# Performance work log

Hardware: AMD Instinct MI355X
Metric: run time of the kernel (lower is better)

Reference implementation:

```python
import jax, jax.numpy as jnp
import numpy as np

B, LQ, LF, NW, NFR, E, D, V = 4, 128, 64, 2, 8, 128, 128, 64


def _project(x, W, b):
    # torch Emb_Projection('linear'): Linear then zero-row mask
    y = x @ W + b
    m = 1.0 - jnp.all(y == 0, axis=-1, keepdims=True).astype(y.dtype)
    return y * m


def setup_inputs() -> dict:
    key = jax.random.key(0)
    ks = jax.random.split(key, 12)
    s = lambda k, shape, fan: jax.random.normal(k, shape, jnp.float32) / np.sqrt(fan)
    return {
        "query": jax.random.normal(ks[0], (B, LQ, E), jnp.float32),
        "fragment": jax.random.normal(ks[1], (B, NW, NFR, LF, E), jnp.float32),
        "query_mask": jnp.ones((B, LQ), jnp.float32),
        "fragment_mask": jnp.ones((B, NW, NFR, LF), jnp.float32),
        # learned params (stored [in, out]; torch Linear is x @ W.T with W [out,in])
        "proj_W": s(ks[2], (E, D), E),
        "proj_b": jnp.zeros((D,), jnp.float32),
        "self_att_W": s(ks[3], (NW, D), D),   # n_way Linear(D,1,bias=False)
        "q_att_W": s(ks[4], (D, V), D),
        "f_att_W": s(ks[5], (D, V), D),
        "qf_att_W": s(ks[6], (D, V), D),
        "gate_w": s(ks[7], (V,), V),          # value_gate: Linear(V,1,bias=False)
        "val_w": s(ks[8], (V,), V),           # value_att:  Linear(V,1,bias=False)
    }


def reference(query, fragment, query_mask, fragment_mask, proj_W, proj_b,
              self_att_W, q_att_W, f_att_W, qf_att_W, gate_w, val_w):
    query = _project(query, proj_W, proj_b)          # [B,Lq,D]
    fragment = _project(fragment, proj_W, proj_b)    # [B,NW,NFR,Lf,D]

    # (1) fragment self-attention -> frag_code
    logits = jnp.einsum('bwfld,wd->bwfl', fragment, self_att_W)   # per-way Linear(D,1)
    e = jnp.exp(logits) * fragment_mask
    frag_self_att = e / (e.sum(-1, keepdims=True) + 1e-7)          # [B,NW,NFR,Lf]
    frag_code = (fragment * frag_self_att[..., None]).sum(-2)     # [B,NW,NFR,D]

    # (2) query-to-fragment attention
    frag_r = fragment.reshape(fragment.shape[0], -1, fragment.shape[-2], fragment.shape[-1])  # [B,NF,Lf,D]
    qr = query[:, None]                                            # [B,1,Lq,D]
    q_att = qr @ q_att_W                                           # [B,1,Lq,V]
    f_att = frag_r @ f_att_W                                       # [B,NF,Lf,V]
    # large broadcast product [B,NF,Lf,Lq,D] then project to V
    qf = (qr[:, :, None, :, :] * frag_r[:, :, :, None, :]) @ qf_att_W  # [B,NF,Lf,Lq,V]
    qf = q_att[:, :, None] + f_att[:, :, :, None] + qf
    qf = qf.max(axis=-3)                                           # max over Lf -> [B,NF,Lq,V]

    qf_gate = jax.nn.sigmoid(qf @ gate_w) * query_mask[:, None]    # [B,NF,Lq]
    e2 = jnp.exp(qf @ val_w) * query_mask[:, None]
    qf_norm = e2 / (e2.sum(-1, keepdims=True) + 1e-7)              # [B,NF,Lq]

    query_code = (qr * qf_norm[..., None]).sum(axis=2)             # [B,NF,D]
    query_code = query_code.reshape(frag_code.shape)               # [B,NW,NFR,D]
    return frag_code, query_code, frag_self_att, qf_gate, query
```

## Files before the change

### kernel.cpp

```cpp
#include <hip/hip_runtime.h>
#include <hip/hip_bf16.h>

#define B_   4
#define LQ_  128
#define LF_  64
#define NW_  2
#define NFR_ 8
#define E_   128
#define D_   128
#define V_   64
#define NWF_ (NW_*NFR_)

using bf16 = __hip_bfloat16;
typedef unsigned short u16;
typedef unsigned int   u32;
typedef __attribute__((ext_vector_type(8))) short  bf16x8;
typedef __attribute__((ext_vector_type(4))) float  f32x4;
typedef __attribute__((ext_vector_type(4))) u32    u32x4;

#define OUT_FRAGCODE  0
#define OUT_QUERYCODE 8192
#define OUT_SELFATT   16384
#define OUT_QFGATE    20480
#define OUT_QUERY     28672

#define L_FP   0
#define L_QP   16384
#define L_FA   49152
#define L_E2   58368
#define L_N    58880
#define L_SAW  59392
#define L_ATT  59904
#define L_RED  60160
#define L_PART 62208
#define L_TOT  62240

__device__ __forceinline__ float us2f(u16 v) { return __uint_as_float((u32)v << 16); }
__device__ __forceinline__ float lo2f(u32 v) { return __uint_as_float(v << 16); }
__device__ __forceinline__ float hi2f(u32 v) { return __uint_as_float(v & 0xffff0000u); }
__device__ __forceinline__ u16 f2b_raw(float f) {
    u32 u = __float_as_uint(f);
    return (u16)((u + 0x7fffu + ((u >> 16) & 1u)) >> 16);
}
__device__ __forceinline__ u32 pk2(float hi, float lo) {
    return __builtin_amdgcn_perm(__float_as_uint(hi), __float_as_uint(lo), 0x07060302u);
}
template<bool BF> __device__ __forceinline__ float LD(const void* p, int i) {
    return BF ? us2f(((const u16*)p)[i]) : ((const float*)p)[i];
}
template<bool BF> __device__ __forceinline__ void ST(void* p, int i, float v) {
    if (BF) ((u16*)p)[i] = f2b_raw(v); else ((float*)p)[i] = v;
}
template<bool BF> __device__ __forceinline__ u16 LDB(const void* p, int i) {
    return BF ? ((const u16*)p)[i] : f2b_raw(((const float*)p)[i]);
}
__device__ __forceinline__ bool is_bf(const void* qmask) {
    return ((const u16*)qmask)[0] == 0x3F80u;
}
template<bool BF>
__device__ __forceinline__ bf16x8 loadA(const void* x, int row, int kt, int quad) {
    int off = row * 128 + kt * 32 + quad * 8;
    if (BF) return *(const bf16x8*)((const u16*)x + off);
    f32x4 a = *(const f32x4*)((const float*)x + off);
    f32x4 c = *(const f32x4*)((const float*)x + off + 4);
    u32x4 av;
    av.x = pk2(a.y, a.x); av.y = pk2(a.w, a.z);
    av.z = pk2(c.y, c.x); av.w = pk2(c.w, c.z);
    return __builtin_bit_cast(bf16x8, av);
}
template<bool BF>
__device__ __forceinline__ bf16x8 ldBf(const void* W, int N, int n, int k0) {
    short tmp[8];
    #pragma unroll
    for (int j = 0; j < 8; ++j) tmp[j] = (short)LDB<BF>(W, (k0 + j) * N + n);
    bf16x8 f;
    #pragma unroll
    for (int j = 0; j < 8; ++j) f[j] = tmp[j];
    return f;
}

template<bool BF>
__device__ __forceinline__ void main_body(
    const void* query, const void* fragment, const void* qmask, const void* fmask,
    const void* projW, const void* projB, const void* saW, const void* qattW,
    const void* fattW, const void* qfW, const void* gatew, const void* valw,
    void* out, char* smem)
{
    u16*   s_fp   = (u16*)(smem + L_FP);
    u16*   s_qp   = (u16*)(smem + L_QP);
    u16*   s_fa   = (u16*)(smem + L_FA);
    float* s_e2   = (float*)(smem + L_E2);
    float* s_n    = (float*)(smem + L_N);
    float* s_saw  = (float*)(smem + L_SAW);
    float* s_att  = (float*)(smem + L_ATT);
    float* s_red  = (float*)(smem + L_RED);
    float* s_part = (float*)(smem + L_PART);

    int bwf = blockIdx.x, b = bwf >> 4;
    int t = threadIdx.x, lane = t & 63, w = t >> 6;
    int m = lane & 15, quad = lane >> 4;
    int sk = (m & 7) << 3;

    {
        bool dofp = (w < 4);
        bf16x8 af_q[4], af_f[4];
        #pragma unroll
        for (int kt = 0; kt < 4; ++kt)
            af_q[kt] = loadA<BF>(query, b * 128 + w * 16 + m, kt, quad);
        if (dofp)
            #pragma unroll
            for (int kt = 0; kt < 4; ++kt)
                af_f[kt] = loadA<BF>(fragment, bwf * 64 + w * 16 + m, kt, quad);
        #pragma unroll
        for (int nt = 0; nt < 8; ++nt) {
            int n = nt * 16 + m;
            bf16x8 bw[4];
            #pragma unroll
            for (int kt = 0; kt < 4; ++kt) bw[kt] = ldBf<BF>(projW, 128, n, kt * 32 + quad * 8);
            float bv = LD<BF>(projB, n);
            f32x4 aq = (f32x4){bv, bv, bv, bv};
            #pragma unroll
            for (int kt = 0; kt < 4; ++kt)
                aq = __builtin_amdgcn_mfma_f32_16x16x32_bf16(af_q[kt], bw[kt], aq, 0, 0, 0);
            #pragma unroll
            for (int rr = 0; rr < 4; ++rr) {
                int row = w * 16 + quad * 4 + rr;
                s_qp[row * 128 + (n ^ ((row & 7) << 3))] = f2b_raw(aq[rr]);
            }
            if (dofp) {
                f32x4 afc = (f32x4){bv, bv, bv, bv};
                #pragma unroll
                for (int kt = 0; kt < 4; ++kt)
                    afc = __builtin_amdgcn_mfma_f32_16x16x32_bf16(af_f[kt], bw[kt], afc, 0, 0, 0);
                #pragma unroll
                for (int rr = 0; rr < 4; ++rr) {
                    int row = w * 16 + quad * 4 + rr;
                    s_fp[row * 128 + (n ^ ((row & 7) << 3))] = f2b_raw(afc[rr]);
                }
            }
        }
    }
    __syncthreads();

    bf16x8 aq2[4];
    #pragma unroll
    for (int kt = 0; kt < 4; ++kt)
        aq2[kt] = *(const bf16x8*)&s_qp[(w * 16 + m) * 128 + ((kt * 32 + quad * 8) ^ sk)];
    f32x4 qat[4];
    #pragma unroll
    for (int vt = 0; vt < 4; ++vt) {
        qat[vt] = (f32x4){0.f, 0.f, 0.f, 0.f};
        #pragma unroll
        for (int kt = 0; kt < 4; ++kt) {
            bf16x8 bb = ldBf<BF>(qattW, 64, vt * 16 + m, kt * 32 + quad * 8);
            qat[vt] = __builtin_amdgcn_mfma_f32_16x16x32_bf16(aq2[kt], bb, qat[vt], 0, 0, 0);
        }
    }
    float qpreg[4][8];
    #pragma unroll
    for (int kt = 0; kt < 4; ++kt) {
        u32x4 uv = __builtin_bit_cast(u32x4, aq2[kt]);
        qpreg[kt][0] = lo2f(uv.x); qpreg[kt][1] = hi2f(uv.x);
        qpreg[kt][2] = lo2f(uv.y); qpreg[kt][3] = hi2f(uv.y);
        qpreg[kt][4] = lo2f(uv.z); qpreg[kt][5] = hi2f(uv.z);
        qpreg[kt][6] = lo2f(uv.w); qpreg[kt][7] = hi2f(uv.w);
    }
    if (w < 4) {
        bf16x8 afa[4];
        #pragma unroll
        for (int kt = 0; kt < 4; ++kt)
            afa[kt] = *(const bf16x8*)&s_fp[(w * 16 + m) * 128 + ((kt * 32 + quad * 8) ^ sk)];
        #pragma unroll
        for (int vt = 0; vt < 4; ++vt) {
            f32x4 a0 = (f32x4){0.f, 0.f, 0.f, 0.f};
            #pragma unroll
            for (int kt = 0; kt < 4; ++kt) {
                bf16x8 wk = ldBf<BF>(fattW, 64, vt * 16 + m, kt * 32 + quad * 8);
                a0 = __builtin_amdgcn_mfma_f32_16x16x32_bf16(afa[kt], wk, a0, 0, 0, 0);
            }
            #pragma unroll
            for (int r = 0; r < 4; ++r)
                s_fa[(w * 16 + quad * 4 + r) * 72 + vt * 16 + m] = f2b_raw(a0[r]);
        }
    }
    bf16x8 w3f[4][4];
    #pragma unroll
    for (int vt = 0; vt < 4; ++vt)
        #pragma unroll
        for (int kt = 0; kt < 4; ++kt)
            w3f[vt][kt] = ldBf<BF>(qfW, 64, vt * 16 + m, kt * 32 + quad * 8);
    __syncthreads();

    float mx[4][4];
    #pragma unroll
    for (int vt = 0; vt < 4; ++vt)
        #pragma unroll
        for (int r = 0; r < 4; ++r) mx[vt][r] = -1e30f;
    #pragma unroll 2
    for (int li = 0; li < 64; ++li) {
        int sw2 = (li & 7) << 3;
        bf16x8 af[4];
        #pragma unroll
        for (int kt = 0; kt < 4; ++kt) {
            u32x4 fv = *(const u32x4*)&s_fp[li * 128 + ((kt * 32 + quad * 8) ^ sw2)];
            u32x4 av;
            av.x = pk2(qpreg[kt][1] * hi2f(fv.x), qpreg[kt][0] * lo2f(fv.x));
            av.y = pk2(qpreg[kt][3] * hi2f(fv.y), qpreg[kt][2] * lo2f(fv.y));
            av.z = pk2(qpreg[kt][5] * hi2f(fv.z), qpreg[kt][4] * lo2f(fv.z));
            av.w = pk2(qpreg[kt][7] * hi2f(fv.w), qpreg[kt][6] * lo2f(fv.w));
            af[kt] = __builtin_bit_cast(bf16x8, av);
        }
        #pragma unroll
        for (int vt = 0; vt < 4; ++vt) {
            float fa = us2f(s_fa[li * 72 + vt * 16 + m]);
            f32x4 acc = (f32x4){fa, fa, fa, fa};
            #pragma unroll
            for (int kt = 0; kt < 4; ++kt)
                acc = __builtin_amdgcn_mfma_f32_16x16x32_bf16(af[kt], w3f[vt][kt], acc, 0, 0, 0);
            #pragma unroll
            for (int r = 0; r < 4; ++r) mx[vt][r] = fmaxf(mx[vt][r], acc[r]);
        }
    }

    {
        float gwv[4], vwv[4];
        #pragma unroll
        for (int vt = 0; vt < 4; ++vt) {
            gwv[vt] = LD<BF>(gatew, vt * 16 + m);
            vwv[vt] = LD<BF>(valw, vt * 16 + m);
        }
        #pragma unroll
        for (int r = 0; r < 4; ++r) {
            float gp = 0.f, ep = 0.f;
            #pragma unroll
            for (int vt = 0; vt < 4; ++vt) {
                float qf = mx[vt][r] + qat[vt][r];
                gp += qf * gwv[vt];
                ep += qf * vwv[vt];
            }
            #pragma unroll
            for (int off = 1; off <= 8; off <<= 1) {
                gp += __shfl_xor(gp, off, 64);
                ep += __shfl_xor(ep, off, 64);
            }
            if (m == 0) {
                int gq = w * 16 + quad * 4 + r;
                float qm = LD<BF>(qmask, b * 128 + gq);
                float g = (1.0f / (1.0f + expf(-gp))) * qm;
                ST<BF>(out, OUT_QFGATE + bwf * LQ_ + gq, g);
                s_e2[gq] = expf(ep) * qm;
            }
        }
    }

    if ((bwf & 15) == 0) {
        #pragma unroll
        for (int it = 0; it < 32; ++it) {
            int i = t + 512 * it;
            int row = i >> 7, col = i & 127;
            float v = us2f(s_qp[row * 128 + (col ^ ((row & 7) << 3))]);
            ST<BF>(out, OUT_QUERY + (b * 128 + row) * 128 + col, v);
        }
    }

    if (t < 128) s_saw[t] = LD<BF>(saW, ((bwf >> 3) & 1) * 128 + t);
    __syncthreads();
    {
        int l = t >> 3, j8 = t & 7;
        int swz = (l & 7) << 3;
        float p = 0.f;
        #pragma unroll
        for (int seg = 0; seg < 2; ++seg) {
            int koff = j8 * 16 + seg * 8;
            u32x4 fv = *(const u32x4*)&s_fp[l * 128 + (koff ^ swz)];
            const float* swp = &s_saw[koff];
            p += lo2f(fv.x) * swp[0] + hi2f(fv.x) * swp[1]
               + lo2f(fv.y) * swp[2] + hi2f(fv.y) * swp[3]
               + lo2f(fv.z) * swp[4] + hi2f(fv.z) * swp[5]
               + lo2f(fv.w) * swp[6] + hi2f(fv.w) * swp[7];
        }
        p += __shfl_xor(p, 1, 64);
        p += __shfl_xor(p, 2, 64);
        p += __shfl_xor(p, 4, 64);
        if (j8 == 0) s_att[l] = expf(p) * LD<BF>(fmask, bwf * LF_ + l);
    }
    __syncthreads();
    if (t < 64) {
        float e = s_att[t], s = e;
        #pragma unroll
        for (int off = 1; off <= 32; off <<= 1) s += __shfl_xor(s, off, 64);
        float nrm = e / (s + 1e-7f);
        s_att[t] = nrm;
        ST<BF>(out, OUT_SELFATT + bwf * LF_ + t, nrm);
    }
    __syncthreads();
    {
        int d = t & 127, grp = t >> 7;
        float fc = 0.f;
        #pragma unroll
        for (int li2 = 0; li2 < 16; ++li2) {
            int l2 = grp * 16 + li2;
            fc += us2f(s_fp[l2 * 128 + (d ^ ((l2 & 7) << 3))]) * s_att[l2];
        }
        s_red[grp * 128 + d] = fc;
    }
    __syncthreads();
    if (t < 128)
        ST<BF>(out, OUT_FRAGCODE + bwf * D_ + t,
               s_red[t] + s_red[128 + t] + s_red[256 + t] + s_red[384 + t]);

    float e2v = 0.f;
    if (t < 128) {
        e2v = s_e2[t];
        float s = e2v;
        #pragma unroll
        for (int off = 1; off <= 32; off <<= 1) s += __shfl_xor(s, off, 64);
        if (lane == 0) s_part[w] = s;
    }
    __syncthreads();
    if (t < 128) {
        float tot = s_part[0] + s_part[1] + 1e-7f;
        s_n[t] = e2v / tot;
    }
    __syncthreads();

    {
        int d = t & 127, qg = t >> 7;
        float qc = 0.f;
        #pragma unroll
        for (int qi = 0; qi < 32; ++qi) {
            int q = qg * 32 + qi;
            qc += us2f(s_qp[q * 128 + (d ^ ((q & 7) << 3))]) * s_n[q];
        }
        s_red[qg * 128 + d] = qc;
    }
    __syncthreads();
    if (t < 128)
        ST<BF>(out, OUT_QUERYCODE + bwf * D_ + t,
               s_red[t] + s_red[128 + t] + s_red[256 + t] + s_red[384 + t]);
}

__global__ __launch_bounds__(512, 2) void k_main(
    const void* query, const void* fragment, const void* qmask, const void* fmask,
    const void* projW, const void* projB, const void* saW, const void* qattW,
    const void* fattW, const void* qfW, const void* gatew, const void* valw,
    void* out)
{
    __shared__ char smem[L_TOT];
    if (is_bf(qmask))
        main_body<true >(query, fragment, qmask, fmask, projW, projB, saW, qattW,
                         fattW, qfW, gatew, valw, out, smem);
    else
        main_body<false>(query, fragment, qmask, fmask, projW, projB, saW, qattW,
                         fattW, qfW, gatew, valw, out, smem);
}

extern "C" void kernel_launch(void* const* d_in, const int* in_sizes, int n_in,
                              void* d_out, int out_size, void* d_ws, size_t ws_size,
                              hipStream_t stream)
{
    hipLaunchKernelGGL(k_main, dim3(B_ * NWF_), dim3(512), 0, stream,
                       d_in[0], d_in[1], d_in[2], d_in[3], d_in[4], d_in[5],
                       d_in[6], d_in[7], d_in[8], d_in[9], d_in[10], d_in[11],
                       d_out);
}
```

Measured before the change: 125.0 us.

## Split query tiles across blocks, pre-transpose weights, add separate query-code kernel

Adds a prep kernel that transposes projection and attention weights into workspace as bf16, so the main kernel loads B fragments contiguously instead of through strided scalar gathers. The main kernel grid grows from 64 to 256 blocks by splitting the 128 queries into four 32-row tiles. Within a block, the Lf max-reduction is split across wave pairs and V halves, then combined through shared memory. The query-code softmax and sum moves into a third kernel that reads e2 and the projected query from workspace. This raises occupancy and parallelism, but adds two extra launches, workspace round trips, and redundant fragment projection in every query tile.

```diff
diff --git a/kernel.cpp b/kernel.cpp
--- a/kernel.cpp
+++ b/kernel.cpp
@@ -18,6 +18,13 @@
 typedef __attribute__((ext_vector_type(4))) float  f32x4;
 typedef __attribute__((ext_vector_type(4))) u32    u32x4;
 
+#define WS_PWT   0
+#define WS_QAT   8192
+#define WS_W3T   12288
+#define WS_WFT   16384
+#define WS_E2    20480
+#define WS_QPB   28672
+
 #define OUT_FRAGCODE  0
 #define OUT_QUERYCODE 8192
 #define OUT_SELFATT   16384
@@ -26,14 +33,12 @@
 
 #define L_FP   0
 #define L_QP   16384
-#define L_FA   49152
-#define L_E2   58368
-#define L_N    58880
-#define L_SAW  59392
-#define L_ATT  59904
-#define L_RED  60160
-#define L_PART 62208
-#define L_TOT  62240
+#define L_FA   24576
+#define L_QAT  33792
+#define L_SAW  38400
+#define L_ATT  38912
+#define L_RED  39168
+#define L_TOT  41216
 
 __device__ __forceinline__ float us2f(u16 v) { return __uint_as_float((u32)v << 16); }
 __device__ __forceinline__ float lo2f(u32 v) { return __uint_as_float(v << 16); }
@@ -68,103 +73,105 @@
     av.z = pk2(c.y, c.x); av.w = pk2(c.w, c.z);
     return __builtin_bit_cast(bf16x8, av);
 }
+
 template<bool BF>
-__device__ __forceinline__ bf16x8 ldBf(const void* W, int N, int n, int k0) {
-    short tmp[8];
-    #pragma unroll
-    for (int j = 0; j < 8; ++j) tmp[j] = (short)LDB<BF>(W, (k0 + j) * N + n);
-    bf16x8 f;
-    #pragma unroll
-    for (int j = 0; j < 8; ++j) f[j] = tmp[j];
-    return f;
+__device__ __forceinline__ void prep_body(const void* src, u16* dst, u16* stg,
+                                          int N, int k0)
+{
+    int t = threadIdx.x, st = N + 1, total = 32 * N;
+    for (int i = t; i < total; i += 256) {
+        int k = i / N, v = i % N;
+        stg[k * st + v] = LDB<BF>(src, (k0 + k) * N + v);
+    }
+    __syncthreads();
+    for (int j = t; j < total; j += 256) {
+        int n = j >> 5, kk = j & 31;
+        dst[n * 128 + k0 + kk] = stg[kk * st + n];
+    }
+}
+__global__ __launch_bounds__(256) void k_prep(
+    const void* projW, const void* qattW, const void* qfW, const void* fattW,
+    const void* qmask, float* ws)
+{
+    __shared__ u16 stg[32 * 129];
+    int mat = blockIdx.x >> 2, kq = blockIdx.x & 3;
+    const void* src = (mat == 0) ? projW : (mat == 1) ? qattW : (mat == 2) ? qfW : fattW;
+    u16* dst = (u16*)(ws + ((mat == 0) ? WS_PWT : (mat == 1) ? WS_QAT : (mat == 2) ? WS_W3T : WS_WFT));
+    int N = (mat == 0) ? 128 : 64;
+    if (is_bf(qmask)) prep_body<true >(src, dst, stg, N, kq * 32);
+    else              prep_body<false>(src, dst, stg, N, kq * 32);
 }
 
 template<bool BF>
 __device__ __forceinline__ void main_body(
     const void* query, const void* fragment, const void* qmask, const void* fmask,
-    const void* projW, const void* projB, const void* saW, const void* qattW,
-    const void* fattW, const void* qfW, const void* gatew, const void* valw,
-    void* out, char* smem)
-{
-    u16*   s_fp   = (u16*)(smem + L_FP);
-    u16*   s_qp   = (u16*)(smem + L_QP);
-    u16*   s_fa   = (u16*)(smem + L_FA);
-    float* s_e2   = (float*)(smem + L_E2);
-    float* s_n    = (float*)(smem + L_N);
-    float* s_saw  = (float*)(smem + L_SAW);
-    float* s_att  = (float*)(smem + L_ATT);
-    float* s_red  = (float*)(smem + L_RED);
-    float* s_part = (float*)(smem + L_PART);
-
-    int bwf = blockIdx.x, b = bwf >> 4;
+    const void* projB, const void* saW, const void* gatew, const void* valw,
+    float* ws, void* out, char* smem)
+{
+    u16*   s_fp  = (u16*)(smem + L_FP);
+    u16*   s_qp  = (u16*)(smem + L_QP);
+    u16*   s_fa  = (u16*)(smem + L_FA);
+    u16*   s_qat = (u16*)(smem + L_QAT);
+    float* s_saw = (float*)(smem + L_SAW);
+    float* s_att = (float*)(smem + L_ATT);
+    float* s_red = (float*)(smem + L_RED);
+
+    int bx = blockIdx.x;
+    int bwf = bx >> 2, qt = bx & 3, b = bwf >> 4;
     int t = threadIdx.x, lane = t & 63, w = t >> 6;
     int m = lane & 15, quad = lane >> 4;
     int sk = (m & 7) << 3;
-
-    {
-        bool dofp = (w < 4);
-        bf16x8 af_q[4], af_f[4];
+    const u16* pwt = (const u16*)(ws + WS_PWT);
+    const u16* qatw = (const u16*)(ws + WS_QAT);
+    const u16* w3t = (const u16*)(ws + WS_W3T);
+    const u16* wft = (const u16*)(ws + WS_WFT);
+
+    if (w < 4) {
+        bf16x8 afr[4];
         #pragma unroll
         for (int kt = 0; kt < 4; ++kt)
-            af_q[kt] = loadA<BF>(query, b * 128 + w * 16 + m, kt, quad);
-        if (dofp)
-            #pragma unroll
-            for (int kt = 0; kt < 4; ++kt)
-                af_f[kt] = loadA<BF>(fragment, bwf * 64 + w * 16 + m, kt, quad);
+            afr[kt] = loadA<BF>(fragment, bwf * 64 + w * 16 + m, kt, quad);
         #pragma unroll
         for (int nt = 0; nt < 8; ++nt) {
             int n = nt * 16 + m;
-            bf16x8 bw[4];
-            #pragma unroll
-            for (int kt = 0; kt < 4; ++kt) bw[kt] = ldBf<BF>(projW, 128, n, kt * 32 + quad * 8);
             float bv = LD<BF>(projB, n);
-            f32x4 aq = (f32x4){bv, bv, bv, bv};
-            #pragma unroll
-            for (int kt = 0; kt < 4; ++kt)
-                aq = __builtin_amdgcn_mfma_f32_16x16x32_bf16(af_q[kt], bw[kt], aq, 0, 0, 0);
+            f32x4 acc = (f32x4){bv, bv, bv, bv};
+            #pragma unroll
+            for (int kt = 0; kt < 4; ++kt) {
+                bf16x8 bw = *(const bf16x8*)(pwt + n * 128 + kt * 32 + quad * 8);
+                acc = __builtin_amdgcn_mfma_f32_16x16x32_bf16(afr[kt], bw, acc, 0, 0, 0);
+            }
             #pragma unroll
             for (int rr = 0; rr < 4; ++rr) {
                 int row = w * 16 + quad * 4 + rr;
-                s_qp[row * 128 + (n ^ ((row & 7) << 3))] = f2b_raw(aq[rr]);
-            }
-            if (dofp) {
-                f32x4 afc = (f32x4){bv, bv, bv, bv};
-                #pragma unroll
-                for (int kt = 0; kt < 4; ++kt)
-                    afc = __builtin_amdgcn_mfma_f32_16x16x32_bf16(af_f[kt], bw[kt], afc, 0, 0, 0);
-                #pragma unroll
-                for (int rr = 0; rr < 4; ++rr) {
-                    int row = w * 16 + quad * 4 + rr;
-                    s_fp[row * 128 + (n ^ ((row & 7) << 3))] = f2b_raw(afc[rr]);
-                }
-            }
-        }
-    }
-    __syncthreads();
-
-    bf16x8 aq2[4];
-    #pragma unroll
-    for (int kt = 0; kt < 4; ++kt)
-        aq2[kt] = *(const bf16x8*)&s_qp[(w * 16 + m) * 128 + ((kt * 32 + quad * 8) ^ sk)];
-    f32x4 qat[4];
-    #pragma unroll
-    for (int vt = 0; vt < 4; ++vt) {
-        qat[vt] = (f32x4){0.f, 0.f, 0.f, 0.f};
-        #pragma unroll
-        for (int kt = 0; kt < 4; ++kt) {
-            bf16x8 bb = ldBf<BF>(qattW, 64, vt * 16 + m, kt * 32 + quad * 8);
-            qat[vt] = __builtin_amdgcn_mfma_f32_16x16x32_bf16(aq2[kt], bb, qat[vt], 0, 0, 0);
-        }
-    }
-    float qpreg[4][8];
-    #pragma unroll
-    for (int kt = 0; kt < 4; ++kt) {
-        u32x4 uv = __builtin_bit_cast(u32x4, aq2[kt]);
-        qpreg[kt][0] = lo2f(uv.x); qpreg[kt][1] = hi2f(uv.x);
-        qpreg[kt][2] = lo2f(uv.y); qpreg[kt][3] = hi2f(uv.y);
-        qpreg[kt][4] = lo2f(uv.z); qpreg[kt][5] = hi2f(uv.z);
-        qpreg[kt][6] = lo2f(uv.w); qpreg[kt][7] = hi2f(uv.w);
-    }
+                s_fp[row * 128 + (n ^ ((row & 7) << 3))] = f2b_raw(acc[rr]);
+            }
+        }
+    } else if (w < 6) {
+        int q0 = (w - 4) * 16;
+        bf16x8 afq[4];
+        #pragma unroll
+        for (int kt = 0; kt < 4; ++kt)
+            afq[kt] = loadA<BF>(query, b * 128 + qt * 32 + q0 + m, kt, quad);
+        #pragma unroll
+        for (int nt = 0; nt < 8; ++nt) {
+            int n = nt * 16 + m;
+            float bv = LD<BF>(projB, n);
+            f32x4 acc = (f32x4){bv, bv, bv, bv};
+            #pragma unroll
+            for (int kt = 0; kt < 4; ++kt) {
+                bf16x8 bw = *(const bf16x8*)(pwt + n * 128 + kt * 32 + quad * 8);
+                acc = __builtin_amdgcn_mfma_f32_16x16x32_bf16(afq[kt], bw, acc, 0, 0, 0);
+            }
+            #pragma unroll
+            for (int rr = 0; rr < 4; ++rr) {
+                int row = q0 + quad * 4 + rr;
+                s_qp[row * 128 + (n ^ ((row & 7) << 3))] = f2b_raw(acc[rr]);
+            }
+        }
+    }
+    __syncthreads();
+
     if (w < 4) {
         bf16x8 afa[4];
         #pragma unroll
@@ -175,34 +182,68 @@
             f32x4 a0 = (f32x4){0.f, 0.f, 0.f, 0.f};
             #pragma unroll
             for (int kt = 0; kt < 4; ++kt) {
-                bf16x8 wk = ldBf<BF>(fattW, 64, vt * 16 + m, kt * 32 + quad * 8);
+                bf16x8 wk = *(const bf16x8*)(wft + (vt * 16 + m) * 128 + kt * 32 + quad * 8);
                 a0 = __builtin_amdgcn_mfma_f32_16x16x32_bf16(afa[kt], wk, a0, 0, 0, 0);
             }
             #pragma unroll
             for (int r = 0; r < 4; ++r)
                 s_fa[(w * 16 + quad * 4 + r) * 72 + vt * 16 + m] = f2b_raw(a0[r]);
         }
-    }
-    bf16x8 w3f[4][4];
+    } else if (w < 6) {
+        int q0 = (w - 4) * 16;
+        bf16x8 aq[4];
+        #pragma unroll
+        for (int kt = 0; kt < 4; ++kt)
+            aq[kt] = *(const bf16x8*)&s_qp[(q0 + m) * 128 + ((kt * 32 + quad * 8) ^ sk)];
+        #pragma unroll
+        for (int vt = 0; vt < 4; ++vt) {
+            f32x4 a0 = (f32x4){0.f, 0.f, 0.f, 0.f};
+            #pragma unroll
+            for (int kt = 0; kt < 4; ++kt) {
+                bf16x8 bk = *(const bf16x8*)(qatw + (vt * 16 + m) * 128 + kt * 32 + quad * 8);
+                a0 = __builtin_amdgcn_mfma_f32_16x16x32_bf16(aq[kt], bk, a0, 0, 0, 0);
+            }
+            #pragma unroll
+            for (int r = 0; r < 4; ++r)
+                s_qat[(q0 + quad * 4 + r) * 72 + vt * 16 + m] = f2b_raw(a0[r]);
+        }
+    }
+    __syncthreads();
+
+    int qsub = w & 1, lhalf = (w >> 1) & 1, vhalf = (w >> 2) & 1;
+    bf16x8 w3f[2][4];
     #pragma unroll
-    for (int vt = 0; vt < 4; ++vt)
+    for (int i = 0; i < 2; ++i)
         #pragma unroll
         for (int kt = 0; kt < 4; ++kt)
-            w3f[vt][kt] = ldBf<BF>(qfW, 64, vt * 16 + m, kt * 32 + quad * 8);
-    __syncthreads();
-
-    float mx[4][4];
+            w3f[i][kt] = *(const bf16x8*)(w3t + ((vhalf * 2 + i) * 16 + m) * 128 + kt * 32 + quad * 8);
+    float qpreg[4][8];
+    {
+        #pragma unroll
+        for (int kt = 0; kt < 4; ++kt) {
+            bf16x8 aq2 = *(const bf16x8*)&s_qp[(qsub * 16 + m) * 128 + ((kt * 32 + quad * 8) ^ sk)];
+            u32x4 uv = __builtin_bit_cast(u32x4, aq2);
+            qpreg[kt][0] = lo2f(uv.x); qpreg[kt][1] = hi2f(uv.x);
+            qpreg[kt][2] = lo2f(uv.y); qpreg[kt][3] = hi2f(uv.y);
+            qpreg[kt][4] = lo2f(uv.z); qpreg[kt][5] = hi2f(uv.z);
+            qpreg[kt][6] = lo2f(uv.w); qpreg[kt][7] = hi2f(uv.w);
+        }
+    }
+    float mx[2][4];
     #pragma unroll
-    for (int vt = 0; vt < 4; ++vt)
-        #pragma unroll
-        for (int r = 0; r < 4; ++r) mx[vt][r] = -1e30f;
+    for (int i = 0; i < 2; ++i)
+        #pragma unroll
+        for (int r = 0; r < 4; ++r) mx[i][r] = -1e30f;
+
+    int lbase = lhalf * 32;
     #pragma unroll 2
-    for (int li = 0; li < 64; ++li) {
-        int sw2 = (li & 7) << 3;
+    for (int li = 0; li < 32; ++li) {
+        int l = lbase + li;
+        int sw = (l & 7) << 3;
         bf16x8 af[4];
         #pragma unroll
         for (int kt = 0; kt < 4; ++kt) {
-            u32x4 fv = *(const u32x4*)&s_fp[li * 128 + ((kt * 32 + quad * 8) ^ sw2)];
+            u32x4 fv = *(const u32x4*)&s_fp[l * 128 + ((kt * 32 + quad * 8) ^ sw)];
             u32x4 av;
             av.x = pk2(qpreg[kt][1] * hi2f(fv.x), qpreg[kt][0] * lo2f(fv.x));
             av.y = pk2(qpreg[kt][3] * hi2f(fv.y), qpreg[kt][2] * lo2f(fv.y));
@@ -211,156 +252,179 @@
             af[kt] = __builtin_bit_cast(bf16x8, av);
         }
         #pragma unroll
-        for (int vt = 0; vt < 4; ++vt) {
-            float fa = us2f(s_fa[li * 72 + vt * 16 + m]);
+        for (int i = 0; i < 2; ++i) {
+            float fa = us2f(s_fa[l * 72 + (vhalf * 2 + i) * 16 + m]);
             f32x4 acc = (f32x4){fa, fa, fa, fa};
             #pragma unroll
             for (int kt = 0; kt < 4; ++kt)
-                acc = __builtin_amdgcn_mfma_f32_16x16x32_bf16(af[kt], w3f[vt][kt], acc, 0, 0, 0);
-            #pragma unroll
-            for (int r = 0; r < 4; ++r) mx[vt][r] = fmaxf(mx[vt][r], acc[r]);
-        }
-    }
+                acc = __builtin_amdgcn_mfma_f32_16x16x32_bf16(af[kt], w3f[i][kt], acc, 0, 0, 0);
+            #pragma unroll
+            for (int r = 0; r < 4; ++r) mx[i][r] = fmaxf(mx[i][r], acc[r]);
+        }
+    }
+    __syncthreads();
+    #pragma unroll
+    for (int i = 0; i < 2; ++i)
+        #pragma unroll
+        for (int r = 0; r < 4; ++r)
+            s_fa[(lhalf * 32 + qsub * 16 + quad * 4 + r) * 72 + (vhalf * 2 + i) * 16 + m] = f2b_raw(mx[i][r]);
+    __syncthreads();
 
     {
-        float gwv[4], vwv[4];
-        #pragma unroll
-        for (int vt = 0; vt < 4; ++vt) {
-            gwv[vt] = LD<BF>(gatew, vt * 16 + m);
-            vwv[vt] = LD<BF>(valw, vt * 16 + m);
-        }
-        #pragma unroll
-        for (int r = 0; r < 4; ++r) {
-            float gp = 0.f, ep = 0.f;
-            #pragma unroll
-            for (int vt = 0; vt < 4; ++vt) {
-                float qf = mx[vt][r] + qat[vt][r];
-                gp += qf * gwv[vt];
-                ep += qf * vwv[vt];
-            }
-            #pragma unroll
-            for (int off = 1; off <= 8; off <<= 1) {
-                gp += __shfl_xor(gp, off, 64);
-                ep += __shfl_xor(ep, off, 64);
-            }
-            if (m == 0) {
-                int gq = w * 16 + quad * 4 + r;
-                float qm = LD<BF>(qmask, b * 128 + gq);
-                float g = (1.0f / (1.0f + expf(-gp))) * qm;
-                ST<BF>(out, OUT_QFGATE + bwf * LQ_ + gq, g);
-                s_e2[gq] = expf(ep) * qm;
-            }
+        int q = t >> 4, vg = t & 15;
+        int gq = qt * 32 + q;
+        float gp = 0.f, ep = 0.f;
+        #pragma unroll
+        for (int jj = 0; jj < 4; ++jj) {
+            int v = vg * 4 + jj;
+            float mval = fmaxf(us2f(s_fa[q * 72 + v]), us2f(s_fa[(32 + q) * 72 + v]));
+            float qf = mval + us2f(s_qat[q * 72 + v]);
+            gp += qf * LD<BF>(gatew, v);
+            ep += qf * LD<BF>(valw, v);
+        }
+        #pragma unroll
+        for (int off = 1; off <= 8; off <<= 1) {
+            gp += __shfl_xor(gp, off, 64);
+            ep += __shfl_xor(ep, off, 64);
+        }
+        if (vg == 0) {
+            float qm = LD<BF>(qmask, b * 128 + gq);
+            float g = (1.0f / (1.0f + expf(-gp))) * qm;
+            ST<BF>(out, OUT_QFGATE + bwf * LQ_ + gq, g);
+            ws[WS_E2 + bwf * 128 + gq] = expf(ep) * qm;
         }
     }
 
     if ((bwf & 15) == 0) {
-        #pragma unroll
-        for (int it = 0; it < 32; ++it) {
+        u16* qpb = (u16*)(ws + WS_QPB);
+        #pragma unroll
+        for (int it = 0; it < 8; ++it) {
             int i = t + 512 * it;
             int row = i >> 7, col = i & 127;
-            float v = us2f(s_qp[row * 128 + (col ^ ((row & 7) << 3))]);
-            ST<BF>(out, OUT_QUERY + (b * 128 + row) * 128 + col, v);
-        }
-    }
-
-    if (t < 128) s_saw[t] = LD<BF>(saW, ((bwf >> 3) & 1) * 128 + t);
-    __syncthreads();
-    {
-        int l = t >> 3, j8 = t & 7;
-        int swz = (l & 7) << 3;
-        float p = 0.f;
-        #pragma unroll
-        for (int seg = 0; seg < 2; ++seg) {
-            int koff = j8 * 16 + seg * 8;
-            u32x4 fv = *(const u32x4*)&s_fp[l * 128 + (koff ^ swz)];
-            const float* swp = &s_saw[koff];
-            p += lo2f(fv.x) * swp[0] + hi2f(fv.x) * swp[1]
-               + lo2f(fv.y) * swp[2] + hi2f(fv.y) * swp[3]
-               + lo2f(fv.z) * swp[4] + hi2f(fv.z) * swp[5]
-               + lo2f(fv.w) * swp[6] + hi2f(fv.w) * swp[7];
-        }
-        p += __shfl_xor(p, 1, 64);
-        p += __shfl_xor(p, 2, 64);
-        p += __shfl_xor(p, 4, 64);
-        if (j8 == 0) s_att[l] = expf(p) * LD<BF>(fmask, bwf * LF_ + l);
-    }
-    __syncthreads();
-    if (t < 64) {
-        float e = s_att[t], s = e;
-        #pragma unroll
-        for (int off = 1; off <= 32; off <<= 1) s += __shfl_xor(s, off, 64);
-        float nrm = e / (s + 1e-7f);
-        s_att[t] = nrm;
-        ST<BF>(out, OUT_SELFATT + bwf * LF_ + t, nrm);
-    }
-    __syncthreads();
-    {
-        int d = t & 127, grp = t >> 7;
-        float fc = 0.f;
-        #pragma unroll
-        for (int li2 = 0; li2 < 16; ++li2) {
-            int l2 = grp * 16 + li2;
-            fc += us2f(s_fp[l2 * 128 + (d ^ ((l2 & 7) << 3))]) * s_att[l2];
-        }
-        s_red[grp * 128 + d] = fc;
-    }
-    __syncthreads();
-    if (t < 128)
-        ST<BF>(out, OUT_FRAGCODE + bwf * D_ + t,
-               s_red[t] + s_red[128 + t] + s_red[256 + t] + s_red[384 + t]);
-
-    float e2v = 0.f;
-    if (t < 128) {
-        e2v = s_e2[t];
-        float s = e2v;
-        #pragma unroll
-        for (int off = 1; off <= 32; off <<= 1) s += __shfl_xor(s, off, 64);
-        if (lane == 0) s_part[w] = s;
-    }
-    __syncthreads();
-    if (t < 128) {
-        float tot = s_part[0] + s_part[1] + 1e-7f;
-        s_n[t] = e2v / tot;
-    }
-    __syncthreads();
-
-    {
-        int d = t & 127, qg = t >> 7;
-        float qc = 0.f;
-        #pragma unroll
-        for (int qi = 0; qi < 32; ++qi) {
-            int q = qg * 32 + qi;
-            qc += us2f(s_qp[q * 128 + (d ^ ((q & 7) << 3))]) * s_n[q];
-        }
-        s_red[qg * 128 + d] = qc;
-    }
-    __syncthreads();
-    if (t < 128)
-        ST<BF>(out, OUT_QUERYCODE + bwf * D_ + t,
-               s_red[t] + s_red[128 + t] + s_red[256 + t] + s_red[384 + t]);
-}
-
-__global__ __launch_bounds__(512, 2) void k_main(
+            u16 raw = s_qp[row * 128 + (col ^ ((row & 7) << 3))];
+            int gr = b * 128 + qt * 32 + row;
+            ST<BF>(out, OUT_QUERY + gr * 128 + col, us2f(raw));
+            qpb[gr * 128 + col] = raw;
+        }
+    }
+
+    if (qt == 0) {
+        if (t < 128) s_saw[t] = LD<BF>(saW, ((bwf >> 3) & 1) * 128 + t);
+        __syncthreads();
+        {
+            int l = t >> 3, j8 = t & 7;
+            int swz = (l & 7) << 3;
+            float p = 0.f;
+            #pragma unroll
+            for (int seg = 0; seg < 2; ++seg) {
+                int koff = j8 * 16 + seg * 8;
+                u32x4 fv = *(const u32x4*)&s_fp[l * 128 + (koff ^ swz)];
+                const float* swp = &s_saw[koff];
+                p += lo2f(fv.x) * swp[0] + hi2f(fv.x) * swp[1]
+                   + lo2f(fv.y) * swp[2] + hi2f(fv.y) * swp[3]
+                   + lo2f(fv.z) * swp[4] + hi2f(fv.z) * swp[5]
+                   + lo2f(fv.w) * swp[6] + hi2f(fv.w) * swp[7];
+            }
+            p += __shfl_xor(p, 1, 64);
+            p += __shfl_xor(p, 2, 64);
+            p += __shfl_xor(p, 4, 64);
+            if (j8 == 0) s_att[l] = expf(p) * LD<BF>(fmask, bwf * LF_ + l);
+        }
+        __syncthreads();
+        if (t < 64) {
+            float e = s_att[t], s = e;
+            #pragma unroll
+            for (int off = 1; off <= 32; off <<= 1) s += __shfl_xor(s, off, 64);
+            float nrm = e / (s + 1e-7f);
+            s_att[t] = nrm;
+            ST<BF>(out, OUT_SELFATT + bwf * LF_ + t, nrm);
+        }
+        __syncthreads();
+        {
+            int d = t & 127, grp = t >> 7;
+            float fc = 0.f;
+            #pragma unroll
+            for (int li2 = 0; li2 < 16; ++li2) {
+                int l2 = grp * 16 + li2;
+                fc += us2f(s_fp[l2 * 128 + (d ^ ((l2 & 7) << 3))]) * s_att[l2];
+            }
+            s_red[grp * 128 + d] = fc;
+        }
+        __syncthreads();
+        if (t < 128)
+            ST<BF>(out, OUT_FRAGCODE + bwf * D_ + t,
+                   s_red[t] + s_red[128 + t] + s_red[256 + t] + s_red[384 + t]);
+    }
+}
+__global__ __launch_bounds__(512, 4) void k_main(
     const void* query, const void* fragment, const void* qmask, const void* fmask,
-    const void* projW, const void* projB, const void* saW, const void* qattW,
-    const void* fattW, const void* qfW, const void* gatew, const void* valw,
-    void* out)
+    const void* projB, const void* saW, const void* gatew, const void* valw,
+    float* ws, void* out)
 {
     __shared__ char smem[L_TOT];
     if (is_bf(qmask))
-        main_body<true >(query, fragment, qmask, fmask, projW, projB, saW, qattW,
-                         fattW, qfW, gatew, valw, out, smem);
+        main_body<true >(query, fragment, qmask, fmask, projB, saW, gatew, valw, ws, out, smem);
     else
-        main_body<false>(query, fragment, qmask, fmask, projW, projB, saW, qattW,
-                         fattW, qfW, gatew, valw, out, smem);
+        main_body<false>(query, fragment, qmask, fmask, projB, saW, gatew, valw, ws, out, smem);
+}
+
+template<bool BF>
+__device__ __forceinline__ void qcode_body(const float* ws, void* out,
+                                           u16* s_q, float* s_n, float* s_part)
+{
+    int bwf = blockIdx.x, b = bwf >> 4, t = threadIdx.x;
+    {
+        const u32* src = (const u32*)((const u16*)(ws + WS_QPB) + (size_t)b * 16384);
+        u32* dst = (u32*)s_q;
+        #pragma unroll
+        for (int it = 0; it < 64; ++it) dst[t + 128 * it] = src[t + 128 * it];
+    }
+    float e = ws[WS_E2 + bwf * 128 + t];
+    float s = e;
+    #pragma unroll
+    for (int off = 1; off <= 32; off <<= 1) s += __shfl_xor(s, off, 64);
+    if ((t & 63) == 0) s_part[t >> 6] = s;
+    __syncthreads();
+    float tot = s_part[0] + s_part[1] + 1e-7f;
+    s_n[t] = e / tot;
+    __syncthreads();
+    float qc = 0.f;
+    #pragma unroll 8
+    for (int q = 0; q < 128; ++q)
+        qc += us2f(s_q[q * 128 + t]) * s_n[q];
+    ST<BF>(out, OUT_QUERYCODE + bwf * D_ + t, qc);
+}
+__global__ __launch_bounds__(128) void k_qcode(const void* qmask, const float* ws, void* out)
+{
+    __shared__ u16 s_q[128 * 128];
+    __shared__ float s_n[128];
+    __shared__ float s_part[2];
+    if (is_bf(qmask)) qcode_body<true >(ws, out, s_q, s_n, s_part);
+    else              qcode_body<false>(ws, out, s_q, s_n, s_part);
 }
 
 extern "C" void kernel_launch(void* const* d_in, const int* in_sizes, int n_in,
                               void* d_out, int out_size, void* d_ws, size_t ws_size,
                               hipStream_t stream)
 {
-    hipLaunchKernelGGL(k_main, dim3(B_ * NWF_), dim3(512), 0, stream,
-                       d_in[0], d_in[1], d_in[2], d_in[3], d_in[4], d_in[5],
-                       d_in[6], d_in[7], d_in[8], d_in[9], d_in[10], d_in[11],
-                       d_out);
-}
+    const void* query    = d_in[0];
+    const void* fragment = d_in[1];
+    const void* qmask    = d_in[2];
+    const void* fmask    = d_in[3];
+    const void* projW    = d_in[4];
+    const void* projB    = d_in[5];
+    const void* saW      = d_in[6];
+    const void* qattW    = d_in[7];
+    const void* fattW    = d_in[8];
+    const void* qfW      = d_in[9];
+    const void* gatew    = d_in[10];
+    const void* valw     = d_in[11];
+    float* ws = (float*)d_ws;
+
+    hipLaunchKernelGGL(k_prep, dim3(16), dim3(256), 0, stream,
+                       projW, qattW, qfW, fattW, qmask, ws);
+    hipLaunchKernelGGL(k_main, dim3(256), dim3(512), 0, stream,
+                       query, fragment, qmask, fmask, projB, saW, gatew, valw, ws, d_out);
+    hipLaunchKernelGGL(k_qcode, dim3(B_ * NWF_), dim3(128), 0, stream,
+                       qmask, ws, d_out);
+}
```

New measurement: 111.8 us. 1.12x faster.
